# Optimization experiments

Hardware: AMD Instinct MI355X
Metric: run time of the kernel (lower is better)

Reference implementation:

```python
import jax, jax.numpy as jnp
import numpy as np

N_NODES = 100000
N_EDGES = 1600000
F_IN = 128
F_HID = 128
F_OUT = 128
N_GRAPHS = 256


def setup_inputs() -> dict:
    key = jax.random.key(0)
    ks = jax.random.split(key, 8)
    x = jax.random.normal(ks[0], (N_NODES, F_IN), dtype=jnp.float32)
    edge_index = jax.random.randint(ks[1], (2, N_EDGES), 0, N_NODES, dtype=jnp.int64)
    batch = jnp.sort(jax.random.randint(ks[2], (N_NODES,), 0, N_GRAPHS, dtype=jnp.int64))
    W1 = jax.random.normal(ks[3], (F_IN, F_HID), dtype=jnp.float32) * 0.05
    b1 = jax.random.normal(ks[4], (F_HID,), dtype=jnp.float32) * 0.05
    W2 = jax.random.normal(ks[5], (F_HID, F_OUT), dtype=jnp.float32) * 0.05
    b2 = jax.random.normal(ks[6], (F_OUT,), dtype=jnp.float32) * 0.05
    return {"x": x, "edge_index": edge_index, "batch": batch,
            "W1": W1, "b1": b1, "W2": W2, "b2": b2}


def reference(x, edge_index, batch, W1, b1, W2, b2):
    n = x.shape[0]
    # --- GCNConv (PyG defaults: add self-loops, symmetric normalization) ---
    loop = jnp.arange(n, dtype=edge_index.dtype)
    row = jnp.concatenate([edge_index[0], loop])  # source nodes
    col = jnp.concatenate([edge_index[1], loop])  # target nodes
    ones = jnp.ones_like(col, dtype=x.dtype)
    deg = jax.ops.segment_sum(ones, col, num_segments=n)          # in-degree incl. self-loop
    dinv = jnp.where(deg > 0, jax.lax.rsqrt(deg), 0.0)
    norm = dinv[row] * dinv[col]                                  # [E+N]
    h = x @ W1                                                    # transform first (PyG order)
    msg = h[row] * norm[:, None]                                  # gather + normalize
    agg = jax.ops.segment_sum(msg, col, num_segments=n) + b1      # scatter-add + bias
    h = jax.nn.relu(agg)
    # --- global_mean_pool over graphs ---
    g_ones = jnp.ones((n,), dtype=x.dtype)
    cnt = jax.ops.segment_sum(g_ones, batch, num_segments=N_GRAPHS)
    pooled = jax.ops.segment_sum(h, batch, num_segments=N_GRAPHS)
    pooled = pooled / jnp.clip(cnt, 1.0)[:, None]
    # --- linear + tanh ---
    return jnp.tanh(pooled @ W2 + b2)
```

## Files before the change

### kernel.cpp

```cpp
#include <hip/hip_runtime.h>
#include <math.h>

#define F 128
#define N_GRAPHS 256
#define BK_SHIFT 8
#define BK_NODES 256
#define BK_CAP 6144
#define MAXBK 512
#define SC_CAP 3200
#define NSCAT 512

typedef __attribute__((ext_vector_type(4))) float f32x4;
typedef __attribute__((ext_vector_type(2))) float f32x2;
typedef __attribute__((ext_vector_type(8))) short bf16x8;
typedef __attribute__((ext_vector_type(8))) unsigned short u16x8;

__device__ __forceinline__ unsigned short f2bf(float f) {
    unsigned u = __float_as_uint(f);
    unsigned r = (u + 0x7FFFu + ((u >> 16) & 1u)) >> 16;
    return (unsigned short)r;
}
__device__ __forceinline__ float bf2f(unsigned short u) {
    return __uint_as_float(((unsigned)u) << 16);
}
__device__ __forceinline__ int idxval(const int* raw, int i, bool is32) {
    return is32 ? raw[i] : (int)((const long long*)raw)[i];
}

#if defined(__has_builtin)
#if __has_builtin(__builtin_amdgcn_cvt_pk_f32_fp8) && __has_builtin(__builtin_amdgcn_cvt_pk_fp8_f32)
#define HW_FP8 1
#endif
#endif

__device__ __forceinline__ unsigned char f2fp8(float f) {
#ifdef HW_FP8
    int p = __builtin_amdgcn_cvt_pk_fp8_f32(f, f, 0, false);
    return (unsigned char)(p & 0xFF);
#else
    float a = fabsf(f);
    unsigned s = (f < 0.f) ? 0x80u : 0u;
    if (a >= 448.f) return s | 0x7E;
    if (a < 0.015625f) {
        int m = (int)(a * 512.f + 0.5f);
        return s | (unsigned)m;
    }
    int ex;
    float fr = frexpf(a, &ex);
    int e = ex - 1;
    int q = (int)(a * exp2f((float)(3 - e)) + 0.5f) - 8;
    if (q == 8) { q = 0; e += 1; }
    return s | ((unsigned)(e + 7) << 3) | (unsigned)q;
#endif
}

__device__ __forceinline__ void fp8x16_fma(uint4 v, float w, float* acc) {
#ifdef HW_FP8
    f32x2 p;
    p = __builtin_amdgcn_cvt_pk_f32_fp8((int)v.x, false); acc[0]  += w * p[0]; acc[1]  += w * p[1];
    p = __builtin_amdgcn_cvt_pk_f32_fp8((int)v.x, true);  acc[2]  += w * p[0]; acc[3]  += w * p[1];
    p = __builtin_amdgcn_cvt_pk_f32_fp8((int)v.y, false); acc[4]  += w * p[0]; acc[5]  += w * p[1];
    p = __builtin_amdgcn_cvt_pk_f32_fp8((int)v.y, true);  acc[6]  += w * p[0]; acc[7]  += w * p[1];
    p = __builtin_amdgcn_cvt_pk_f32_fp8((int)v.z, false); acc[8]  += w * p[0]; acc[9]  += w * p[1];
    p = __builtin_amdgcn_cvt_pk_f32_fp8((int)v.z, true);  acc[10] += w * p[0]; acc[11] += w * p[1];
    p = __builtin_amdgcn_cvt_pk_f32_fp8((int)v.w, false); acc[12] += w * p[0]; acc[13] += w * p[1];
    p = __builtin_amdgcn_cvt_pk_f32_fp8((int)v.w, true);  acc[14] += w * p[0]; acc[15] += w * p[1];
#else
    unsigned ww[4] = {v.x, v.y, v.z, v.w};
#pragma unroll
    for (int j = 0; j < 16; ++j) {
        unsigned b = (ww[j >> 2] >> ((j & 3) * 8)) & 0xFF;
        int e = (b >> 3) & 0xF, m = b & 7;
        float val = e ? ldexpf((float)(8 + m), e - 10) : ldexpf((float)m, -9);
        acc[j] += (b & 0x80) ? -(w * val) : (w * val);
    }
#endif
}

__global__ __launch_bounds__(256) void w1t_kernel(
    const float* __restrict__ W1, unsigned short* __restrict__ W1T) {
    int i = blockIdx.x * 256 + threadIdx.x;
    int k = i >> 7, n = i & 127;
    W1T[n * F + k] = f2bf(W1[i]);
}

__global__ __launch_bounds__(256) void scatter_gemm_kernel(
    const int* __restrict__ ei_raw, int nE,
    const int* __restrict__ batch_raw, int nN,
    const float* __restrict__ x, const unsigned short* __restrict__ W1T,
    unsigned char* __restrict__ h_f8,
    int* __restrict__ bcursor, int* __restrict__ tmp, int nBk) {
    extern __shared__ char smem[];
    int t = threadIdx.x;

    if (blockIdx.x < NSCAT) {
        int2* ebuf  = (int2*)smem;
        int*  hist  = (int*)(smem + SC_CAP * 8);
        int*  rbase = hist + MAXBK;
        bool is32 = (batch_raw[nN - 1] != 0);
        int cs = (nE + NSCAT - 1) / NSCAT;
        int e0 = blockIdx.x * cs;
        int e1 = min(nE, e0 + cs);

        for (int s0 = e0; s0 < e1; s0 += SC_CAP) {
            int m = min(SC_CAP, e1 - s0);
            for (int i = t; i < nBk; i += 256) hist[i] = 0;
            __syncthreads();
            for (int i = t; i < m; i += 256) {
                int r = idxval(ei_raw, s0 + i, is32);
                int c = idxval(ei_raw, nE + s0 + i, is32);
                ebuf[i] = make_int2(r, c);
                atomicAdd(&hist[c >> BK_SHIFT], 1);
            }
            __syncthreads();
            for (int i = t; i < nBk; i += 256) {
                int hv = hist[i];
                rbase[i] = hv ? (i * BK_CAP + atomicAdd(&bcursor[i], hv)) : 0;
                hist[i] = 0;
            }
            __syncthreads();
            for (int i = t; i < m; i += 256) {
                int2 e = ebuf[i];
                int b = e.y >> BK_SHIFT;
                int pos = rbase[b] + atomicAdd(&hist[b], 1);
                if (pos < (b + 1) * BK_CAP)
                    tmp[pos] = e.x | ((e.y & (BK_NODES - 1)) << 20);
            }
            __syncthreads();
        }
    } else {
        unsigned short* xs = (unsigned short*)smem;
        int row0 = (blockIdx.x - NSCAT) * 128;

#pragma unroll
        for (int j = 0; j < 16; ++j) {
            int idx = t + j * 256;
            int r = idx >> 5, c4 = idx & 31;
            int gr = row0 + r;
            float4 v = make_float4(0.f, 0.f, 0.f, 0.f);
            if (gr < nN) v = ((const float4*)x)[(size_t)gr * 32 + c4];
            ushort4 o;
            o.x = f2bf(v.x); o.y = f2bf(v.y); o.z = f2bf(v.z); o.w = f2bf(v.w);
            int byte = (r * 256 + c4 * 8) ^ ((r & 7) << 4);
            *(ushort4*)((char*)xs + byte) = o;
        }
        __syncthreads();

        int lane = t & 63;
        int w = t >> 6;
        int m0 = (w >> 1) * 64;
        int n0 = (w & 1) * 64;
        int l15 = lane & 15;
        int lg = lane >> 4;

        f32x4 acc[4][4] = {};
#pragma unroll
        for (int ks = 0; ks < 4; ++ks) {
            bf16x8 a[4], b[4];
#pragma unroll
            for (int i = 0; i < 4; ++i) {
                int r = m0 + i * 16 + l15;
                int byte = (r * 256 + ks * 64 + lg * 16) ^ ((r & 7) << 4);
                a[i] = *(const bf16x8*)((const char*)xs + byte);
            }
#pragma unroll
            for (int j = 0; j < 4; ++j) {
                int n = n0 + j * 16 + l15;
                b[j] = *(const bf16x8*)(W1T + (size_t)n * F + ks * 32 + lg * 8);
            }
#pragma unroll
            for (int i = 0; i < 4; ++i)
#pragma unroll
                for (int j = 0; j < 4; ++j)
                    acc[i][j] = __builtin_amdgcn_mfma_f32_16x16x32_bf16(
                        a[i], b[j], acc[i][j], 0, 0, 0);
        }

#pragma unroll
        for (int i = 0; i < 4; ++i) {
#pragma unroll
            for (int r = 0; r < 4; ++r) {
                int gm = row0 + m0 + i * 16 + lg * 4 + r;
                if (gm < nN) {
#pragma unroll
                    for (int j = 0; j < 4; ++j) {
                        int n = n0 + j * 16 + l15;
                        h_f8[(size_t)gm * F + n] = f2fp8(acc[i][j][r]);
                    }
                }
            }
        }
    }
}

__global__ __launch_bounds__(256) void bucket_build_kernel(
    const int* __restrict__ tmp, const int* __restrict__ bfill, int nN,
    int* __restrict__ off, int* __restrict__ cnt, float* __restrict__ dinv,
    int* __restrict__ csr) {
    __shared__ int ebuf[BK_CAP];
    __shared__ int h[BK_NODES];
    __shared__ int pfx[BK_NODES];
    __shared__ int lcur[BK_NODES];
    int b = blockIdx.x;
    int t = threadIdx.x;
    int nodeLo = b << BK_SHIFT;
    int base = b * BK_CAP;
    int m = min(bfill[b], BK_CAP);

    h[t] = 0;
    for (int i = t; i < m; i += 256) ebuf[i] = tmp[base + i];
    __syncthreads();
    for (int i = t; i < m; i += 256)
        atomicAdd(&h[ebuf[i] >> 20], 1);
    __syncthreads();
    int own = h[t];
    int pad = (own + 3) & ~3;
    pfx[t] = pad;
    __syncthreads();
    for (int st = 1; st < 256; st <<= 1) {
        int add = (t >= st) ? pfx[t - st] : 0;
        __syncthreads();
        pfx[t] += add;
        __syncthreads();
    }
    int myoff = base + pfx[t] - pad;
    lcur[t] = myoff;
    int node = nodeLo + t;
    if (node < nN) {
        off[node] = myoff;
        cnt[node] = own;
        dinv[node] = rsqrtf((float)(own + 1));
    }
    __syncthreads();
    for (int i = t; i < m; i += 256) {
        int e = ebuf[i];
        int pos = atomicAdd(&lcur[e >> 20], 1);
        csr[pos] = e & 0xFFFFF;
    }
}

__global__ __launch_bounds__(256) void aggregate_kernel(
    const unsigned char* __restrict__ h_f8, const int* __restrict__ csr,
    const int* __restrict__ off, const int* __restrict__ cnt,
    const float* __restrict__ dinv, const float* __restrict__ b1,
    unsigned short* __restrict__ agg_bf, int nN) {
    int t = threadIdx.x;
    int lane = t & 7;
    int c = blockIdx.x * 32 + (t >> 3);
    if (c >= nN) return;

    const uint4* h4 = (const uint4*)h_f8;
    int n = cnt[c];
    float dc = rsqrtf((float)(n + 1));
    float acc[16];
#pragma unroll
    for (int j = 0; j < 16; ++j) acc[j] = 0.f;
    fp8x16_fma(h4[(size_t)c * 8 + lane], dc, acc);

    int lo = off[c];
    int k = 0;
    for (; k + 4 <= n; k += 4) {
        int4 e = *(const int4*)(csr + lo + k);
        float w0 = dinv[e.x];
        float w1 = dinv[e.y];
        float w2 = dinv[e.z];
        float w3 = dinv[e.w];
        uint4 v0 = h4[(size_t)e.x * 8 + lane];
        uint4 v1 = h4[(size_t)e.y * 8 + lane];
        uint4 v2 = h4[(size_t)e.z * 8 + lane];
        uint4 v3 = h4[(size_t)e.w * 8 + lane];
        fp8x16_fma(v0, w0, acc);
        fp8x16_fma(v1, w1, acc);
        fp8x16_fma(v2, w2, acc);
        fp8x16_fma(v3, w3, acc);
    }
    if (k < n) {
        int4 e = *(const int4*)(csr + lo + k);
        fp8x16_fma(h4[(size_t)e.x * 8 + lane], dinv[e.x], acc);
        if (k + 1 < n) fp8x16_fma(h4[(size_t)e.y * 8 + lane], dinv[e.y], acc);
        if (k + 2 < n) fp8x16_fma(h4[(size_t)e.z * 8 + lane], dinv[e.z], acc);
    }

    const float* b1p = b1 + lane * 16;
    u16x8 r0, r1;
#pragma unroll
    for (int j = 0; j < 8; ++j) {
        r0[j] = f2bf(fmaxf(b1p[j] + dc * acc[j], 0.f));
        r1[j] = f2bf(fmaxf(b1p[8 + j] + dc * acc[8 + j], 0.f));
    }
    *(u16x8*)(agg_bf + (size_t)c * F + lane * 16) = r0;
    *(u16x8*)(agg_bf + (size_t)c * F + lane * 16 + 8) = r1;
}

__global__ __launch_bounds__(256) void pool_final_kernel(
    const unsigned short* __restrict__ agg_bf,
    const int* __restrict__ batch_raw, int nN,
    const float* __restrict__ W2, const float* __restrict__ b2,
    float* __restrict__ out) {
    int g = blockIdx.x;
    bool is32 = (batch_raw[nN - 1] != 0);
    __shared__ int bounds[2];
    __shared__ float sd[16][F];
    __shared__ float ps[F];
    int t = threadIdx.x;
    if (t < 2) {
        int target = g + t;
        int lo = 0, hi = nN;
        while (lo < hi) {
            int mid = (lo + hi) >> 1;
            if (idxval(batch_raw, mid, is32) < target) lo = mid + 1; else hi = mid;
        }
        bounds[t] = lo;
    }
    __syncthreads();
    int lo = bounds[0], hi = bounds[1];

    int lane = t & 15;
    int grp = t >> 4;
    const u16x8* a8 = (const u16x8*)agg_bf;
    float acc[8];
#pragma unroll
    for (int j = 0; j < 8; ++j) acc[j] = 0.f;
    for (int n = lo + grp; n < hi; n += 16) {
        u16x8 v = a8[(size_t)n * 16 + lane];
#pragma unroll
        for (int j = 0; j < 8; ++j) acc[j] += bf2f(v[j]);
    }
#pragma unroll
    for (int j = 0; j < 8; ++j) sd[grp][lane * 8 + j] = acc[j];
    __syncthreads();

    if (t < F) {
        float s = 0.f;
#pragma unroll
        for (int i = 0; i < 16; ++i) s += sd[i][t];
        float cntf = (float)(hi - lo);
        ps[t] = s / fmaxf(cntf, 1.0f);
    }
    __syncthreads();

    if (t < F) {
        float s = b2[t];
        for (int k = 0; k < F; ++k) s += ps[k] * W2[k * F + t];
        out[g * F + t] = tanhf(s);
    }
}

extern "C" void kernel_launch(void* const* d_in, const int* in_sizes, int n_in,
                              void* d_out, int out_size, void* d_ws, size_t ws_size,
                              hipStream_t stream) {
    const float* x     = (const float*)d_in[0];
    const int*   ei    = (const int*)d_in[1];
    const int*   batch = (const int*)d_in[2];
    const float* W1    = (const float*)d_in[3];
    const float* b1    = (const float*)d_in[4];
    const float* W2    = (const float*)d_in[5];
    const float* b2    = (const float*)d_in[6];
    float* out = (float*)d_out;

    const int nN = in_sizes[2];
    const int nE = in_sizes[1] / 2;
    const int nBk = (nN + BK_NODES - 1) >> BK_SHIFT;
    const int nGemm = (nN + 127) / 128;

    char* ws = (char*)d_ws;
    size_t woff = 0;
    auto take = [&](size_t bytes) {
        void* p = ws + woff;
        woff += (bytes + 15) & ~(size_t)15;
        return p;
    };
    unsigned char*  h_f8   = (unsigned char*)take((size_t)nN * F);
    unsigned short* agg_bf = (unsigned short*)take((size_t)nN * F * 2);
    int*   tmp      = (int*)take((size_t)nBk * BK_CAP * 4);
    int*   csr      = (int*)take((size_t)nBk * BK_CAP * 4);
    int*   cnt      = (int*)take((size_t)nN * 4);
    int*   off      = (int*)take((size_t)nN * 4);
    float* dinv     = (float*)take((size_t)nN * 4);
    unsigned short* W1T = (unsigned short*)take((size_t)F * F * 2);
    int*   bcursor  = (int*)take((size_t)nBk * 4);

    hipMemsetAsync(bcursor, 0, (size_t)nBk * 4, stream);
    w1t_kernel<<<F * F / 256, 256, 0, stream>>>(W1, W1T);
    scatter_gemm_kernel<<<NSCAT + nGemm, 256, 32768, stream>>>(
        ei, nE, batch, nN, x, W1T, h_f8, bcursor, tmp, nBk);
    bucket_build_kernel<<<nBk, 256, 0, stream>>>(tmp, bcursor, nN, off, cnt,
                                                 dinv, csr);
    aggregate_kernel<<<(nN + 31) / 32, 256, 0, stream>>>(h_f8, csr, off, cnt,
                                                         dinv, b1, agg_bf, nN);
    pool_final_kernel<<<N_GRAPHS, 256, 0, stream>>>(agg_bf, batch, nN, W2, b2, out);
}
```

Baseline: 122.7 us.

## Pair GEMM with bucket build instead of scatter, split scatter into own kernel

Moves the x@W1 GEMM blocks out of the scatter kernel and into the same launch as the bucket-build (CSR construction) blocks. Scatter now runs alone with twice as many blocks and half the per-chunk shared buffer. The aim is to overlap the GEMM with the CSR build rather than with the edge scatter and to spread scatter atomics across more blocks. The bucket-build blocks now take 32 KB of dynamic shared memory, the GEMM's allocation, which may lower their occupancy.

```diff
diff --git a/kernel.cpp b/kernel.cpp
--- a/kernel.cpp
+++ b/kernel.cpp
@@ -7,8 +7,8 @@
 #define BK_NODES 256
 #define BK_CAP 6144
 #define MAXBK 512
-#define SC_CAP 3200
-#define NSCAT 512
+#define SC_CAP 1600
+#define NSCAT 1024
 
 typedef __attribute__((ext_vector_type(4))) float f32x4;
 typedef __attribute__((ext_vector_type(2))) float f32x2;
@@ -84,53 +84,99 @@
     W1T[n * F + k] = f2bf(W1[i]);
 }
 
-__global__ __launch_bounds__(256) void scatter_gemm_kernel(
+__global__ __launch_bounds__(256) void scatter_kernel(
     const int* __restrict__ ei_raw, int nE,
     const int* __restrict__ batch_raw, int nN,
+    int* __restrict__ bcursor, int* __restrict__ tmp, int nBk) {
+    __shared__ int2 ebuf[SC_CAP];
+    __shared__ int hist[MAXBK];
+    __shared__ int rbase[MAXBK];
+    int t = threadIdx.x;
+    bool is32 = (batch_raw[nN - 1] != 0);
+    int cs = (nE + gridDim.x - 1) / gridDim.x;
+    int e0 = blockIdx.x * cs;
+    int e1 = min(nE, e0 + cs);
+
+    for (int s0 = e0; s0 < e1; s0 += SC_CAP) {
+        int m = min(SC_CAP, e1 - s0);
+        for (int i = t; i < nBk; i += 256) hist[i] = 0;
+        __syncthreads();
+        for (int i = t; i < m; i += 256) {
+            int r = idxval(ei_raw, s0 + i, is32);
+            int c = idxval(ei_raw, nE + s0 + i, is32);
+            ebuf[i] = make_int2(r, c);
+            atomicAdd(&hist[c >> BK_SHIFT], 1);
+        }
+        __syncthreads();
+        for (int i = t; i < nBk; i += 256) {
+            int hv = hist[i];
+            rbase[i] = hv ? (i * BK_CAP + atomicAdd(&bcursor[i], hv)) : 0;
+            hist[i] = 0;
+        }
+        __syncthreads();
+        for (int i = t; i < m; i += 256) {
+            int2 e = ebuf[i];
+            int b = e.y >> BK_SHIFT;
+            int pos = rbase[b] + atomicAdd(&hist[b], 1);
+            if (pos < (b + 1) * BK_CAP)
+                tmp[pos] = e.x | ((e.y & (BK_NODES - 1)) << 20);
+        }
+        __syncthreads();
+    }
+}
+
+__global__ __launch_bounds__(256) void gemm_build_kernel(
     const float* __restrict__ x, const unsigned short* __restrict__ W1T,
+    const int* __restrict__ tmp, const int* __restrict__ bfill, int nN,
     unsigned char* __restrict__ h_f8,
-    int* __restrict__ bcursor, int* __restrict__ tmp, int nBk) {
+    int* __restrict__ off, int* __restrict__ cnt, float* __restrict__ dinv,
+    int* __restrict__ csr, int nBk) {
     extern __shared__ char smem[];
     int t = threadIdx.x;
 
-    if (blockIdx.x < NSCAT) {
-        int2* ebuf  = (int2*)smem;
-        int*  hist  = (int*)(smem + SC_CAP * 8);
-        int*  rbase = hist + MAXBK;
-        bool is32 = (batch_raw[nN - 1] != 0);
-        int cs = (nE + NSCAT - 1) / NSCAT;
-        int e0 = blockIdx.x * cs;
-        int e1 = min(nE, e0 + cs);
-
-        for (int s0 = e0; s0 < e1; s0 += SC_CAP) {
-            int m = min(SC_CAP, e1 - s0);
-            for (int i = t; i < nBk; i += 256) hist[i] = 0;
+    if (blockIdx.x < (unsigned)nBk) {
+        int* ebuf = (int*)smem;
+        int* h    = ebuf + BK_CAP;
+        int* pfx  = h + BK_NODES;
+        int* lcur = pfx + BK_NODES;
+        int b = blockIdx.x;
+        int nodeLo = b << BK_SHIFT;
+        int base = b * BK_CAP;
+        int m = min(bfill[b], BK_CAP);
+
+        h[t] = 0;
+        for (int i = t; i < m; i += 256) ebuf[i] = tmp[base + i];
+        __syncthreads();
+        for (int i = t; i < m; i += 256)
+            atomicAdd(&h[ebuf[i] >> 20], 1);
+        __syncthreads();
+        int own = h[t];
+        int pad = (own + 3) & ~3;
+        pfx[t] = pad;
+        __syncthreads();
+        for (int st = 1; st < 256; st <<= 1) {
+            int add = (t >= st) ? pfx[t - st] : 0;
             __syncthreads();
-            for (int i = t; i < m; i += 256) {
-                int r = idxval(ei_raw, s0 + i, is32);
-                int c = idxval(ei_raw, nE + s0 + i, is32);
-                ebuf[i] = make_int2(r, c);
-                atomicAdd(&hist[c >> BK_SHIFT], 1);
-            }
+            pfx[t] += add;
             __syncthreads();
-            for (int i = t; i < nBk; i += 256) {
-                int hv = hist[i];
-                rbase[i] = hv ? (i * BK_CAP + atomicAdd(&bcursor[i], hv)) : 0;
-                hist[i] = 0;
-            }
-            __syncthreads();
-            for (int i = t; i < m; i += 256) {
-                int2 e = ebuf[i];
-                int b = e.y >> BK_SHIFT;
-                int pos = rbase[b] + atomicAdd(&hist[b], 1);
-                if (pos < (b + 1) * BK_CAP)
-                    tmp[pos] = e.x | ((e.y & (BK_NODES - 1)) << 20);
-            }
-            __syncthreads();
+        }
+        int myoff = base + pfx[t] - pad;
+        lcur[t] = myoff;
+        int node = nodeLo + t;
+        if (node < nN) {
+            off[node] = myoff;
+            cnt[node] = own;
+            dinv[node] = rsqrtf((float)(own + 1));
+        }
+        __syncthreads();
+        for (int i = t; i < m; i += 256) {
+            int e = ebuf[i];
+            int pos = atomicAdd(&lcur[e >> 20], 1);
+            csr[pos] = e & 0xFFFFF;
         }
     } else {
         unsigned short* xs = (unsigned short*)smem;
-        int row0 = (blockIdx.x - NSCAT) * 128;
+        int row0 = (blockIdx.x - nBk) * 128;
 
 #pragma unroll
         for (int j = 0; j < 16; ++j) {
@@ -190,52 +236,6 @@
                 }
             }
         }
-    }
-}
-
-__global__ __launch_bounds__(256) void bucket_build_kernel(
-    const int* __restrict__ tmp, const int* __restrict__ bfill, int nN,
-    int* __restrict__ off, int* __restrict__ cnt, float* __restrict__ dinv,
-    int* __restrict__ csr) {
-    __shared__ int ebuf[BK_CAP];
-    __shared__ int h[BK_NODES];
-    __shared__ int pfx[BK_NODES];
-    __shared__ int lcur[BK_NODES];
-    int b = blockIdx.x;
-    int t = threadIdx.x;
-    int nodeLo = b << BK_SHIFT;
-    int base = b * BK_CAP;
-    int m = min(bfill[b], BK_CAP);
-
-    h[t] = 0;
-    for (int i = t; i < m; i += 256) ebuf[i] = tmp[base + i];
-    __syncthreads();
-    for (int i = t; i < m; i += 256)
-        atomicAdd(&h[ebuf[i] >> 20], 1);
-    __syncthreads();
-    int own = h[t];
-    int pad = (own + 3) & ~3;
-    pfx[t] = pad;
-    __syncthreads();
-    for (int st = 1; st < 256; st <<= 1) {
-        int add = (t >= st) ? pfx[t - st] : 0;
-        __syncthreads();
-        pfx[t] += add;
-        __syncthreads();
-    }
-    int myoff = base + pfx[t] - pad;
-    lcur[t] = myoff;
-    int node = nodeLo + t;
-    if (node < nN) {
-        off[node] = myoff;
-        cnt[node] = own;
-        dinv[node] = rsqrtf((float)(own + 1));
-    }
-    __syncthreads();
-    for (int i = t; i < m; i += 256) {
-        int e = ebuf[i];
-        int pos = atomicAdd(&lcur[e >> 20], 1);
-        csr[pos] = e & 0xFFFFF;
     }
 }
 
@@ -382,10 +382,9 @@
 
     hipMemsetAsync(bcursor, 0, (size_t)nBk * 4, stream);
     w1t_kernel<<<F * F / 256, 256, 0, stream>>>(W1, W1T);
-    scatter_gemm_kernel<<<NSCAT + nGemm, 256, 32768, stream>>>(
-        ei, nE, batch, nN, x, W1T, h_f8, bcursor, tmp, nBk);
-    bucket_build_kernel<<<nBk, 256, 0, stream>>>(tmp, bcursor, nN, off, cnt,
-                                                 dinv, csr);
+    scatter_kernel<<<NSCAT, 256, 0, stream>>>(ei, nE, batch, nN, bcursor, tmp, nBk);
+    gemm_build_kernel<<<nBk + nGemm, 256, 32768, stream>>>(
+        x, W1T, tmp, bcursor, nN, h_f8, off, cnt, dinv, csr, nBk);
     aggregate_kernel<<<(nN + 31) / 32, 256, 0, stream>>>(h_f8, csr, off, cnt,
                                                          dinv, b1, agg_bf, nN);
     pool_final_kernel<<<N_GRAPHS, 256, 0, stream>>>(agg_bf, batch, nN, W2, b2, out);
```

Result: slower. 133.7 us (+9.0%).

## Fuse mean-pool into aggregation and interleave scatter/GEMM blocks

Applied to the files above, without the earlier changes.

The aggregation kernel now reduces post-ReLU node features straight into per-graph sums, using shared-memory partials for the few graphs a 32-node block covers and global float atomics otherwise. This removes the bf16 intermediate write and the separate pass that read it back for pooling. The final kernel only normalizes and applies W2 and tanh. The scatter and GEMM blocks in the first kernel are also interleaved 2:3, so the memory-bound scatter and the MFMA GEMM run concurrently rather than in order. In exchange it adds shared and global atomic traffic, and float atomics make the summation order nondeterministic.

```diff
diff --git a/kernel.cpp b/kernel.cpp
--- a/kernel.cpp
+++ b/kernel.cpp
@@ -9,6 +9,7 @@
 #define MAXBK 512
 #define SC_CAP 3200
 #define NSCAT 512
+#define GSPAN 8
 
 typedef __attribute__((ext_vector_type(4))) float f32x4;
 typedef __attribute__((ext_vector_type(2))) float f32x2;
@@ -89,17 +90,21 @@
     const int* __restrict__ batch_raw, int nN,
     const float* __restrict__ x, const unsigned short* __restrict__ W1T,
     unsigned char* __restrict__ h_f8,
-    int* __restrict__ bcursor, int* __restrict__ tmp, int nBk) {
+    int* __restrict__ bcursor, int* __restrict__ tmp, int nBk, int nGemm) {
     extern __shared__ char smem[];
     int t = threadIdx.x;
-
-    if (blockIdx.x < NSCAT) {
+    int q = blockIdx.x / 5;
+    int r5 = blockIdx.x % 5;
+
+    if (r5 < 2) {
+        int sb = q * 2 + r5;
+        if (sb >= NSCAT) return;
         int2* ebuf  = (int2*)smem;
         int*  hist  = (int*)(smem + SC_CAP * 8);
         int*  rbase = hist + MAXBK;
         bool is32 = (batch_raw[nN - 1] != 0);
         int cs = (nE + NSCAT - 1) / NSCAT;
-        int e0 = blockIdx.x * cs;
+        int e0 = sb * cs;
         int e1 = min(nE, e0 + cs);
 
         for (int s0 = e0; s0 < e1; s0 += SC_CAP) {
@@ -107,10 +112,10 @@
             for (int i = t; i < nBk; i += 256) hist[i] = 0;
             __syncthreads();
             for (int i = t; i < m; i += 256) {
-                int r = idxval(ei_raw, s0 + i, is32);
-                int c = idxval(ei_raw, nE + s0 + i, is32);
-                ebuf[i] = make_int2(r, c);
-                atomicAdd(&hist[c >> BK_SHIFT], 1);
+                int rr = idxval(ei_raw, s0 + i, is32);
+                int cc = idxval(ei_raw, nE + s0 + i, is32);
+                ebuf[i] = make_int2(rr, cc);
+                atomicAdd(&hist[cc >> BK_SHIFT], 1);
             }
             __syncthreads();
             for (int i = t; i < nBk; i += 256) {
@@ -129,19 +134,21 @@
             __syncthreads();
         }
     } else {
+        int gb = q * 3 + (r5 - 2);
+        if (gb >= nGemm) return;
         unsigned short* xs = (unsigned short*)smem;
-        int row0 = (blockIdx.x - NSCAT) * 128;
+        int row0 = gb * 128;
 
 #pragma unroll
         for (int j = 0; j < 16; ++j) {
             int idx = t + j * 256;
-            int r = idx >> 5, c4 = idx & 31;
-            int gr = row0 + r;
+            int rr = idx >> 5, c4 = idx & 31;
+            int gr = row0 + rr;
             float4 v = make_float4(0.f, 0.f, 0.f, 0.f);
             if (gr < nN) v = ((const float4*)x)[(size_t)gr * 32 + c4];
             ushort4 o;
             o.x = f2bf(v.x); o.y = f2bf(v.y); o.z = f2bf(v.z); o.w = f2bf(v.w);
-            int byte = (r * 256 + c4 * 8) ^ ((r & 7) << 4);
+            int byte = (rr * 256 + c4 * 8) ^ ((rr & 7) << 4);
             *(ushort4*)((char*)xs + byte) = o;
         }
         __syncthreads();
@@ -159,8 +166,8 @@
             bf16x8 a[4], b[4];
 #pragma unroll
             for (int i = 0; i < 4; ++i) {
-                int r = m0 + i * 16 + l15;
-                int byte = (r * 256 + ks * 64 + lg * 16) ^ ((r & 7) << 4);
+                int rr = m0 + i * 16 + l15;
+                int byte = (rr * 256 + ks * 64 + lg * 16) ^ ((rr & 7) << 4);
                 a[i] = *(const bf16x8*)((const char*)xs + byte);
             }
 #pragma unroll
@@ -179,13 +186,13 @@
 #pragma unroll
         for (int i = 0; i < 4; ++i) {
 #pragma unroll
-            for (int r = 0; r < 4; ++r) {
-                int gm = row0 + m0 + i * 16 + lg * 4 + r;
+            for (int rr = 0; rr < 4; ++rr) {
+                int gm = row0 + m0 + i * 16 + lg * 4 + rr;
                 if (gm < nN) {
 #pragma unroll
                     for (int j = 0; j < 4; ++j) {
                         int n = n0 + j * 16 + l15;
-                        h_f8[(size_t)gm * F + n] = f2fp8(acc[i][j][r]);
+                        h_f8[(size_t)gm * F + n] = f2fp8(acc[i][j][rr]);
                     }
                 }
             }
@@ -239,68 +246,104 @@
     }
 }
 
-__global__ __launch_bounds__(256) void aggregate_kernel(
+__global__ __launch_bounds__(256) void aggregate_pool_kernel(
     const unsigned char* __restrict__ h_f8, const int* __restrict__ csr,
     const int* __restrict__ off, const int* __restrict__ cnt,
     const float* __restrict__ dinv, const float* __restrict__ b1,
-    unsigned short* __restrict__ agg_bf, int nN) {
+    const int* __restrict__ batch_raw, float* __restrict__ pooled, int nN) {
+    __shared__ float part[GSPAN][F];
+    __shared__ int ginfo[2];
     int t = threadIdx.x;
     int lane = t & 7;
     int c = blockIdx.x * 32 + (t >> 3);
-    if (c >= nN) return;
-
-    const uint4* h4 = (const uint4*)h_f8;
-    int n = cnt[c];
-    float dc = rsqrtf((float)(n + 1));
-    float acc[16];
-#pragma unroll
-    for (int j = 0; j < 16; ++j) acc[j] = 0.f;
-    fp8x16_fma(h4[(size_t)c * 8 + lane], dc, acc);
-
-    int lo = off[c];
-    int k = 0;
-    for (; k + 4 <= n; k += 4) {
-        int4 e = *(const int4*)(csr + lo + k);
-        float w0 = dinv[e.x];
-        float w1 = dinv[e.y];
-        float w2 = dinv[e.z];
-        float w3 = dinv[e.w];
-        uint4 v0 = h4[(size_t)e.x * 8 + lane];
-        uint4 v1 = h4[(size_t)e.y * 8 + lane];
-        uint4 v2 = h4[(size_t)e.z * 8 + lane];
-        uint4 v3 = h4[(size_t)e.w * 8 + lane];
-        fp8x16_fma(v0, w0, acc);
-        fp8x16_fma(v1, w1, acc);
-        fp8x16_fma(v2, w2, acc);
-        fp8x16_fma(v3, w3, acc);
-    }
-    if (k < n) {
-        int4 e = *(const int4*)(csr + lo + k);
-        fp8x16_fma(h4[(size_t)e.x * 8 + lane], dinv[e.x], acc);
-        if (k + 1 < n) fp8x16_fma(h4[(size_t)e.y * 8 + lane], dinv[e.y], acc);
-        if (k + 2 < n) fp8x16_fma(h4[(size_t)e.z * 8 + lane], dinv[e.z], acc);
+    bool valid = (c < nN);
+    bool is32 = (batch_raw[nN - 1] != 0);
+
+    int c0 = blockIdx.x * 32;
+    if (t == 0) {
+        int cLast = min(c0 + 31, nN - 1);
+        int g0 = idxval(batch_raw, c0, is32);
+        int g1 = idxval(batch_raw, cLast, is32);
+        ginfo[0] = g0;
+        ginfo[1] = g1 - g0 + 1;
+    }
+    for (int i = t; i < GSPAN * F; i += 256) ((float*)part)[i] = 0.f;
+    __syncthreads();
+    int g0 = ginfo[0], span = ginfo[1];
+
+    float accv[16];
+#pragma unroll
+    for (int j = 0; j < 16; ++j) accv[j] = 0.f;
+    int myg = 0;
+    float dc = 0.f;
+
+    if (valid) {
+        const uint4* h4 = (const uint4*)h_f8;
+        int n = cnt[c];
+        dc = rsqrtf((float)(n + 1));
+        fp8x16_fma(h4[(size_t)c * 8 + lane], dc, accv);
+
+        int lo = off[c];
+        int k = 0;
+        for (; k + 4 <= n; k += 4) {
+            int4 e = *(const int4*)(csr + lo + k);
+            float w0 = dinv[e.x];
+            float w1 = dinv[e.y];
+            float w2 = dinv[e.z];
+            float w3 = dinv[e.w];
+            uint4 v0 = h4[(size_t)e.x * 8 + lane];
+            uint4 v1 = h4[(size_t)e.y * 8 + lane];
+            uint4 v2 = h4[(size_t)e.z * 8 + lane];
+            uint4 v3 = h4[(size_t)e.w * 8 + lane];
+            fp8x16_fma(v0, w0, accv);
+            fp8x16_fma(v1, w1, accv);
+            fp8x16_fma(v2, w2, accv);
+            fp8x16_fma(v3, w3, accv);
+        }
+        if (k < n) {
+            int4 e = *(const int4*)(csr + lo + k);
+            fp8x16_fma(h4[(size_t)e.x * 8 + lane], dinv[e.x], accv);
+            if (k + 1 < n) fp8x16_fma(h4[(size_t)e.y * 8 + lane], dinv[e.y], accv);
+            if (k + 2 < n) fp8x16_fma(h4[(size_t)e.z * 8 + lane], dinv[e.z], accv);
+        }
+        myg = idxval(batch_raw, c, is32);
     }
 
     const float* b1p = b1 + lane * 16;
-    u16x8 r0, r1;
-#pragma unroll
-    for (int j = 0; j < 8; ++j) {
-        r0[j] = f2bf(fmaxf(b1p[j] + dc * acc[j], 0.f));
-        r1[j] = f2bf(fmaxf(b1p[8 + j] + dc * acc[8 + j], 0.f));
-    }
-    *(u16x8*)(agg_bf + (size_t)c * F + lane * 16) = r0;
-    *(u16x8*)(agg_bf + (size_t)c * F + lane * 16 + 8) = r1;
-}
-
-__global__ __launch_bounds__(256) void pool_final_kernel(
-    const unsigned short* __restrict__ agg_bf,
-    const int* __restrict__ batch_raw, int nN,
-    const float* __restrict__ W2, const float* __restrict__ b2,
+    if (valid) {
+        int gl = myg - g0;
+        if (span <= GSPAN) {
+#pragma unroll
+            for (int j = 0; j < 16; ++j) {
+                float v = fmaxf(b1p[j] + dc * accv[j], 0.f);
+                atomicAdd(&part[gl][lane * 16 + j], v);
+            }
+        } else {
+#pragma unroll
+            for (int j = 0; j < 16; ++j) {
+                float v = fmaxf(b1p[j] + dc * accv[j], 0.f);
+                atomicAdd(&pooled[myg * F + lane * 16 + j], v);
+            }
+        }
+    }
+    __syncthreads();
+
+    if (span <= GSPAN) {
+        for (int i = t; i < span * F; i += 256) {
+            float v = ((float*)part)[i];
+            if (v != 0.f)
+                atomicAdd(&pooled[(g0 + (i >> 7)) * F + (i & (F - 1))], v);
+        }
+    }
+}
+
+__global__ __launch_bounds__(128) void final_kernel(
+    const float* __restrict__ pooled, const int* __restrict__ batch_raw,
+    int nN, const float* __restrict__ W2, const float* __restrict__ b2,
     float* __restrict__ out) {
     int g = blockIdx.x;
     bool is32 = (batch_raw[nN - 1] != 0);
     __shared__ int bounds[2];
-    __shared__ float sd[16][F];
     __shared__ float ps[F];
     int t = threadIdx.x;
     if (t < 2) {
@@ -313,37 +356,13 @@
         bounds[t] = lo;
     }
     __syncthreads();
-    int lo = bounds[0], hi = bounds[1];
-
-    int lane = t & 15;
-    int grp = t >> 4;
-    const u16x8* a8 = (const u16x8*)agg_bf;
-    float acc[8];
-#pragma unroll
-    for (int j = 0; j < 8; ++j) acc[j] = 0.f;
-    for (int n = lo + grp; n < hi; n += 16) {
-        u16x8 v = a8[(size_t)n * 16 + lane];
-#pragma unroll
-        for (int j = 0; j < 8; ++j) acc[j] += bf2f(v[j]);
-    }
-#pragma unroll
-    for (int j = 0; j < 8; ++j) sd[grp][lane * 8 + j] = acc[j];
-    __syncthreads();
-
-    if (t < F) {
-        float s = 0.f;
-#pragma unroll
-        for (int i = 0; i < 16; ++i) s += sd[i][t];
-        float cntf = (float)(hi - lo);
-        ps[t] = s / fmaxf(cntf, 1.0f);
-    }
-    __syncthreads();
-
-    if (t < F) {
-        float s = b2[t];
-        for (int k = 0; k < F; ++k) s += ps[k] * W2[k * F + t];
-        out[g * F + t] = tanhf(s);
-    }
+    float cntf = (float)(bounds[1] - bounds[0]);
+    ps[t] = pooled[g * F + t] / fmaxf(cntf, 1.0f);
+    __syncthreads();
+
+    float s = b2[t];
+    for (int k = 0; k < F; ++k) s += ps[k] * W2[k * F + t];
+    out[g * F + t] = tanhf(s);
 }
 
 extern "C" void kernel_launch(void* const* d_in, const int* in_sizes, int n_in,
@@ -362,6 +381,10 @@
     const int nE = in_sizes[1] / 2;
     const int nBk = (nN + BK_NODES - 1) >> BK_SHIFT;
     const int nGemm = (nN + 127) / 128;
+    int nQ = (NSCAT + 1) / 2;
+    int nQg = (nGemm + 2) / 3;
+    if (nQg > nQ) nQ = nQg;
+    const int gridA = nQ * 5;
 
     char* ws = (char*)d_ws;
     size_t woff = 0;
@@ -370,23 +393,23 @@
         woff += (bytes + 15) & ~(size_t)15;
         return p;
     };
-    unsigned char*  h_f8   = (unsigned char*)take((size_t)nN * F);
-    unsigned short* agg_bf = (unsigned short*)take((size_t)nN * F * 2);
+    unsigned char*  h_f8 = (unsigned char*)take((size_t)nN * F);
     int*   tmp      = (int*)take((size_t)nBk * BK_CAP * 4);
     int*   csr      = (int*)take((size_t)nBk * BK_CAP * 4);
     int*   cnt      = (int*)take((size_t)nN * 4);
     int*   off      = (int*)take((size_t)nN * 4);
     float* dinv     = (float*)take((size_t)nN * 4);
     unsigned short* W1T = (unsigned short*)take((size_t)F * F * 2);
-    int*   bcursor  = (int*)take((size_t)nBk * 4);
-
-    hipMemsetAsync(bcursor, 0, (size_t)nBk * 4, stream);
+    int*   bcursor  = (int*)take((size_t)(nBk + N_GRAPHS * F) * 4);
+    float* pooled   = (float*)(bcursor + nBk);
+
+    hipMemsetAsync(bcursor, 0, (size_t)(nBk + N_GRAPHS * F) * 4, stream);
     w1t_kernel<<<F * F / 256, 256, 0, stream>>>(W1, W1T);
-    scatter_gemm_kernel<<<NSCAT + nGemm, 256, 32768, stream>>>(
-        ei, nE, batch, nN, x, W1T, h_f8, bcursor, tmp, nBk);
+    scatter_gemm_kernel<<<gridA, 256, 32768, stream>>>(
+        ei, nE, batch, nN, x, W1T, h_f8, bcursor, tmp, nBk, nGemm);
     bucket_build_kernel<<<nBk, 256, 0, stream>>>(tmp, bcursor, nN, off, cnt,
                                                  dinv, csr);
-    aggregate_kernel<<<(nN + 31) / 32, 256, 0, stream>>>(h_f8, csr, off, cnt,
-                                                         dinv, b1, agg_bf, nN);
-    pool_final_kernel<<<N_GRAPHS, 256, 0, stream>>>(agg_bf, batch, nN, W2, b2, out);
-}
+    aggregate_pool_kernel<<<(nN + 31) / 32, 256, 0, stream>>>(
+        h_f8, csr, off, cnt, dinv, b1, batch, pooled, nN);
+    final_kernel<<<N_GRAPHS, 128, 0, stream>>>(pooled, batch, nN, W2, b2, out);
+}
```

Measured after the change: 167.8 us. 36.8% more time.

## Interleave scatter and GEMM blocks, halve GEMM tile, stream edges without LDS buffer

Applied to the files above, without the earlier changes.

The fused scatter/GEMM kernel now interleaves one scatter block with six GEMM blocks across the grid, so both kinds of work are spread over the CUs from the start instead of all scatter blocks running first. GEMM tiles shrink from 128 to 64 rows, and shared memory drops to 16KB to allow higher occupancy. Scatter blocks are halved to 256 and no longer stage edges in LDS. Each block now reads the edge list twice from global memory, once for the histogram and once for the placement, which adds global traffic.

```diff
diff --git a/kernel.cpp b/kernel.cpp
--- a/kernel.cpp
+++ b/kernel.cpp
@@ -7,8 +7,7 @@
 #define BK_NODES 256
 #define BK_CAP 6144
 #define MAXBK 512
-#define SC_CAP 3200
-#define NSCAT 512
+#define NSCAT 256
 
 typedef __attribute__((ext_vector_type(4))) float f32x4;
 typedef __attribute__((ext_vector_type(2))) float f32x2;
@@ -89,78 +88,78 @@
     const int* __restrict__ batch_raw, int nN,
     const float* __restrict__ x, const unsigned short* __restrict__ W1T,
     unsigned char* __restrict__ h_f8,
-    int* __restrict__ bcursor, int* __restrict__ tmp, int nBk) {
+    int* __restrict__ bcursor, int* __restrict__ tmp, int nBk, int nGemm) {
     extern __shared__ char smem[];
     int t = threadIdx.x;
-
-    if (blockIdx.x < NSCAT) {
-        int2* ebuf  = (int2*)smem;
-        int*  hist  = (int*)(smem + SC_CAP * 8);
-        int*  rbase = hist + MAXBK;
+    int q = blockIdx.x / 7;
+    int r7 = blockIdx.x % 7;
+
+    if (r7 == 0) {
+        int sb = q;
+        if (sb >= NSCAT) return;
+        int* hist  = (int*)smem;
+        int* rbase = hist + MAXBK;
         bool is32 = (batch_raw[nN - 1] != 0);
         int cs = (nE + NSCAT - 1) / NSCAT;
-        int e0 = blockIdx.x * cs;
+        int e0 = sb * cs;
         int e1 = min(nE, e0 + cs);
 
-        for (int s0 = e0; s0 < e1; s0 += SC_CAP) {
-            int m = min(SC_CAP, e1 - s0);
-            for (int i = t; i < nBk; i += 256) hist[i] = 0;
-            __syncthreads();
-            for (int i = t; i < m; i += 256) {
-                int r = idxval(ei_raw, s0 + i, is32);
-                int c = idxval(ei_raw, nE + s0 + i, is32);
-                ebuf[i] = make_int2(r, c);
-                atomicAdd(&hist[c >> BK_SHIFT], 1);
-            }
-            __syncthreads();
-            for (int i = t; i < nBk; i += 256) {
-                int hv = hist[i];
-                rbase[i] = hv ? (i * BK_CAP + atomicAdd(&bcursor[i], hv)) : 0;
-                hist[i] = 0;
-            }
-            __syncthreads();
-            for (int i = t; i < m; i += 256) {
-                int2 e = ebuf[i];
-                int b = e.y >> BK_SHIFT;
-                int pos = rbase[b] + atomicAdd(&hist[b], 1);
-                if (pos < (b + 1) * BK_CAP)
-                    tmp[pos] = e.x | ((e.y & (BK_NODES - 1)) << 20);
-            }
-            __syncthreads();
+        for (int i = t; i < nBk; i += 256) hist[i] = 0;
+        __syncthreads();
+        for (int e = e0 + t; e < e1; e += 256) {
+            int c = idxval(ei_raw, nE + e, is32);
+            atomicAdd(&hist[c >> BK_SHIFT], 1);
+        }
+        __syncthreads();
+        for (int i = t; i < nBk; i += 256) {
+            int hv = hist[i];
+            rbase[i] = hv ? (i * BK_CAP + atomicAdd(&bcursor[i], hv)) : 0;
+            hist[i] = 0;
+        }
+        __syncthreads();
+        for (int e = e0 + t; e < e1; e += 256) {
+            int r = idxval(ei_raw, e, is32);
+            int c = idxval(ei_raw, nE + e, is32);
+            int b = c >> BK_SHIFT;
+            int pos = rbase[b] + atomicAdd(&hist[b], 1);
+            if (pos < (b + 1) * BK_CAP)
+                tmp[pos] = r | ((c & (BK_NODES - 1)) << 20);
         }
     } else {
+        int gb = q * 6 + (r7 - 1);
+        if (gb >= nGemm) return;
         unsigned short* xs = (unsigned short*)smem;
-        int row0 = (blockIdx.x - NSCAT) * 128;
-
-#pragma unroll
-        for (int j = 0; j < 16; ++j) {
+        int row0 = gb * 64;
+
+#pragma unroll
+        for (int j = 0; j < 8; ++j) {
             int idx = t + j * 256;
-            int r = idx >> 5, c4 = idx & 31;
-            int gr = row0 + r;
+            int rr = idx >> 5, c4 = idx & 31;
+            int gr = row0 + rr;
             float4 v = make_float4(0.f, 0.f, 0.f, 0.f);
             if (gr < nN) v = ((const float4*)x)[(size_t)gr * 32 + c4];
             ushort4 o;
             o.x = f2bf(v.x); o.y = f2bf(v.y); o.z = f2bf(v.z); o.w = f2bf(v.w);
-            int byte = (r * 256 + c4 * 8) ^ ((r & 7) << 4);
+            int byte = (rr * 256 + c4 * 8) ^ ((rr & 7) << 4);
             *(ushort4*)((char*)xs + byte) = o;
         }
         __syncthreads();
 
         int lane = t & 63;
         int w = t >> 6;
-        int m0 = (w >> 1) * 64;
+        int m0 = (w >> 1) * 32;
         int n0 = (w & 1) * 64;
         int l15 = lane & 15;
         int lg = lane >> 4;
 
-        f32x4 acc[4][4] = {};
+        f32x4 acc[2][4] = {};
 #pragma unroll
         for (int ks = 0; ks < 4; ++ks) {
-            bf16x8 a[4], b[4];
-#pragma unroll
-            for (int i = 0; i < 4; ++i) {
-                int r = m0 + i * 16 + l15;
-                int byte = (r * 256 + ks * 64 + lg * 16) ^ ((r & 7) << 4);
+            bf16x8 a[2], b[4];
+#pragma unroll
+            for (int i = 0; i < 2; ++i) {
+                int rr = m0 + i * 16 + l15;
+                int byte = (rr * 256 + ks * 64 + lg * 16) ^ ((rr & 7) << 4);
                 a[i] = *(const bf16x8*)((const char*)xs + byte);
             }
 #pragma unroll
@@ -169,7 +168,7 @@
                 b[j] = *(const bf16x8*)(W1T + (size_t)n * F + ks * 32 + lg * 8);
             }
 #pragma unroll
-            for (int i = 0; i < 4; ++i)
+            for (int i = 0; i < 2; ++i)
 #pragma unroll
                 for (int j = 0; j < 4; ++j)
                     acc[i][j] = __builtin_amdgcn_mfma_f32_16x16x32_bf16(
@@ -177,15 +176,15 @@
         }
 
 #pragma unroll
-        for (int i = 0; i < 4; ++i) {
-#pragma unroll
-            for (int r = 0; r < 4; ++r) {
-                int gm = row0 + m0 + i * 16 + lg * 4 + r;
+        for (int i = 0; i < 2; ++i) {
+#pragma unroll
+            for (int rr = 0; rr < 4; ++rr) {
+                int gm = row0 + m0 + i * 16 + lg * 4 + rr;
                 if (gm < nN) {
 #pragma unroll
                     for (int j = 0; j < 4; ++j) {
                         int n = n0 + j * 16 + l15;
-                        h_f8[(size_t)gm * F + n] = f2fp8(acc[i][j][r]);
+                        h_f8[(size_t)gm * F + n] = f2fp8(acc[i][j][rr]);
                     }
                 }
             }
@@ -361,7 +360,11 @@
     const int nN = in_sizes[2];
     const int nE = in_sizes[1] / 2;
     const int nBk = (nN + BK_NODES - 1) >> BK_SHIFT;
-    const int nGemm = (nN + 127) / 128;
+    const int nGemm = (nN + 63) / 64;
+    int nQ = NSCAT;
+    int nQg = (nGemm + 5) / 6;
+    if (nQg > nQ) nQ = nQg;
+    const int gridA = nQ * 7;
 
     char* ws = (char*)d_ws;
     size_t woff = 0;
@@ -382,8 +385,8 @@
 
     hipMemsetAsync(bcursor, 0, (size_t)nBk * 4, stream);
     w1t_kernel<<<F * F / 256, 256, 0, stream>>>(W1, W1T);
-    scatter_gemm_kernel<<<NSCAT + nGemm, 256, 32768, stream>>>(
-        ei, nE, batch, nN, x, W1T, h_f8, bcursor, tmp, nBk);
+    scatter_gemm_kernel<<<gridA, 256, 16384, stream>>>(
+        ei, nE, batch, nN, x, W1T, h_f8, bcursor, tmp, nBk, nGemm);
     bucket_build_kernel<<<nBk, 256, 0, stream>>>(tmp, bcursor, nN, off, cnt,
                                                  dinv, csr);
     aggregate_kernel<<<(nN + 31) / 32, 256, 0, stream>>>(h_f8, csr, off, cnt,
```

New measurement: 130.1 us. 1.06x slower.
